# Kernel optimization log

Hardware: AMD Instinct MI355X
Metric: run time of the kernel (lower is better)

The kernel has to match this reference:

```python
import jax, jax.numpy as jnp
import numpy as np

N_HEADS = 16


def setup_inputs() -> dict:
    key = jax.random.key(0)
    k1, k2, k3 = jax.random.split(key, 3)
    d = 1024
    x = jax.random.normal(k1, (8, 1024, d), dtype=jnp.float32)
    w_qkv = jax.random.normal(k2, (d, 3 * d), dtype=jnp.float32) * (1.0 / np.sqrt(d))
    w_out = jax.random.normal(k3, (d, d), dtype=jnp.float32) * (1.0 / np.sqrt(d))
    b_out = jnp.zeros((d,), dtype=jnp.float32)
    return {"x": x, "w_qkv": w_qkv, "w_out": w_out, "b_out": b_out}


def reference(x, w_qkv, w_out, b_out):
    a, b, c = x.shape
    h = N_HEADS
    hd = c // h
    scale = 1.0 / (c ** 0.5)  # note: 1/sqrt(model_dim), not head_dim
    qkv = (x @ w_qkv).reshape(a, b, 3, h, hd)
    q, k, v = jnp.moveaxis(qkv, 2, 0)          # each (a, b, h, hd)
    q = jnp.swapaxes(q, 1, 2)                  # (a, h, b, hd)
    k = jnp.swapaxes(k, 1, 2)
    v = jnp.swapaxes(v, 1, 2)
    scores = jnp.einsum('ahqd,ahkd->ahqk', q, k) * scale  # (a, h, b, b)
    # Faithful to the source: softmax over dim=1 (the HEADS axis)
    attn = jax.nn.softmax(scores, axis=1)
    out = jnp.einsum('ahqk,ahkd->ahqd', attn, v)           # (a, h, b, hd)
    out = jnp.swapaxes(out, 1, 2).reshape(a, b, c)
    return out @ w_out + b_out
```

## Files before the change

kernel.cpp:

```cpp
#include <hip/hip_runtime.h>
#include <hip/hip_bf16.h>

typedef __attribute__((ext_vector_type(8))) short short8;
typedef __attribute__((ext_vector_type(4))) float f32x4;
typedef __attribute__((ext_vector_type(16))) float f32x16;
typedef __attribute__((ext_vector_type(4))) unsigned uint4v;

#define SC_LOG2E 0.04508422f
#define MFMA32(a, b, c) __builtin_amdgcn_mfma_f32_32x32x16_bf16(a, b, c, 0, 0, 0)

__device__ inline short bf16r(float f) {
    union { float f; unsigned u; } v; v.f = f;
    unsigned r = v.u + 0x7FFFu + ((v.u >> 16) & 1u);
    return (short)(r >> 16);
}
__device__ inline float bflo(unsigned u) {
    union { unsigned u; float f; } v; v.u = u << 16; return v.f;
}
__device__ inline float bfhi(unsigned u) {
    union { unsigned u; float f; } v; v.u = u & 0xffff0000u; return v.f;
}
#if __has_builtin(__builtin_amdgcn_exp2f)
__device__ inline float fexp2(float x) { return __builtin_amdgcn_exp2f(x); }
#else
__device__ inline float fexp2(float x) { return __expf(x * 0.6931471806f); }
#endif
__device__ inline unsigned cvt_pk_bf16(float lo, float hi) {
    unsigned r;
    asm("v_cvt_pk_bf16_f32 %0, %1, %2" : "=v"(r) : "v"(lo), "v"(hi));
    return r;
}
__device__ inline void perm32swap(unsigned& a, unsigned& b) {
    asm("v_permlane32_swap_b32 %0, %1" : "+v"(a), "+v"(b));
}

#define GLOAD_LDS16(gp, lp) __builtin_amdgcn_global_load_lds( \
    (const __attribute__((address_space(1))) unsigned int*)(gp), \
    (__attribute__((address_space(3))) unsigned int*)(lp), 16, 0, 0)

__global__ void castk(const float* __restrict__ in, short* __restrict__ out, int n4) {
    int i = blockIdx.x * 256 + threadIdx.x;
    if (i < n4) {
        float4 v = ((const float4*)in)[i];
        short4 o;
        o.x = bf16r(v.x); o.y = bf16r(v.y); o.z = bf16r(v.z); o.w = bf16r(v.w);
        ((short4*)out)[i] = o;
    }
}

__global__ void tcast(const float* __restrict__ src, short* __restrict__ dst, int R, int C,
                      int nscale, float sfac) {
    __shared__ float tile[32][33];
    int bi = blockIdx.x, bj = blockIdx.y;
    int tx = threadIdx.x & 31, ty = threadIdx.x >> 5;
#pragma unroll
    for (int p = 0; p < 4; p++)
        tile[ty + p * 8][tx] = src[(long)(bi * 32 + ty + p * 8) * C + bj * 32 + tx];
    __syncthreads();
#pragma unroll
    for (int p = 0; p < 4; p++) {
        int n = bj * 32 + ty + p * 8;
        float v = tile[tx][ty + p * 8];
        if (n < nscale) v *= sfac;
        dst[(long)n * R + bi * 32 + tx] = bf16r(v);
    }
}

__global__ void vtrans(const short* __restrict__ qkv, short* __restrict__ Vt) {
    __shared__ short tile[32][33];
    int a = blockIdx.z, bi = blockIdx.x, bj = blockIdx.y;
    int tx = threadIdx.x & 31, ty = threadIdx.x >> 5;
#pragma unroll
    for (int p = 0; p < 4; p++) {
        int k = bi * 32 + ty + p * 8;
        int r = bj * 32 + tx;
        tile[ty + p * 8][tx] = qkv[(long)(a * 1024 + k) * 3072 + 2048 + r];
    }
    __syncthreads();
#pragma unroll
    for (int p = 0; p < 4; p++) {
        int r = bj * 32 + ty + p * 8;
        int k = bi * 32 + tx;
        Vt[(long)a * 1048576 + (long)r * 1024 + k] = tile[tx][ty + p * 8];
    }
}

template<int OUT_BF16>
__global__ __launch_bounds__(256, 2)
void gemm_bt(const short* __restrict__ A, const short* __restrict__ Bt,
             void* __restrict__ Cout, const float* __restrict__ bias,
             int M, int N, int K, int nbx, int cpx, int lda) {
    __shared__ short As[2][128 * 32];
    __shared__ short Bs[2][128 * 32];
    const int wg = blockIdx.x;
    const int lg = (wg & 7) * cpx + (wg >> 3);
    const int bx = lg % nbx, by = lg / nbx;
    const int tid = threadIdx.x, w = tid >> 6, lane = tid & 63;
    const int wr = w >> 1, wc = w & 1;
    const int l15 = lane & 15, lhi = lane >> 4;
    const int m0 = by * 128, n0 = bx * 128;
    f32x4 acc[4][4] = {};
    const int NT = K / 32;

    auto stage = [&](int buf, int t) {
        int k0 = t * 32;
#pragma unroll
        for (int j = 0; j < 2; j++) {
            int chunk = w * 128 + j * 64 + lane;
            int row = chunk >> 2, cc = chunk & 3;
            GLOAD_LDS16(A  + (long)(m0 + row) * lda + k0 + cc * 8, &As[buf][chunk * 8]);
            GLOAD_LDS16(Bt + (long)(n0 + row) * K   + k0 + cc * 8, &Bs[buf][chunk * 8]);
        }
    };

    stage(0, 0);
    __syncthreads();
    int buf = 0;
    for (int t = 0; t < NT; t++) {
        if (t + 1 < NT) stage(buf ^ 1, t + 1);
        short8 af[4], bfr[4];
#pragma unroll
        for (int i = 0; i < 4; i++) {
            af[i]  = *(const short8*)(&As[buf][(wr * 64 + i * 16 + l15) * 32 + lhi * 8]);
            bfr[i] = *(const short8*)(&Bs[buf][(wc * 64 + i * 16 + l15) * 32 + lhi * 8]);
        }
#pragma unroll
        for (int i = 0; i < 4; i++)
#pragma unroll
            for (int j = 0; j < 4; j++)
                acc[i][j] = __builtin_amdgcn_mfma_f32_16x16x32_bf16(af[i], bfr[j], acc[i][j], 0, 0, 0);
        __syncthreads();
        buf ^= 1;
    }
#pragma unroll
    for (int i = 0; i < 4; i++)
#pragma unroll
        for (int j = 0; j < 4; j++)
#pragma unroll
            for (int r = 0; r < 4; r++) {
                int row = m0 + wr * 64 + i * 16 + lhi * 4 + r;
                int col = n0 + wc * 64 + j * 16 + l15;
                float v = acc[i][j][r];
                if (OUT_BF16) ((short*)Cout)[(long)row * N + col] = bf16r(v);
                else          ((float*)Cout)[(long)row * N + col] = v + bias[col];
            }
}

__global__ __launch_bounds__(256, 2)
void dsum_kernel(const short* __restrict__ qkv, unsigned* __restrict__ negL) {
    __shared__ short Qs[2][128 * 64];
    __shared__ short Ks[2][128 * 64];
    const int wg = blockIdx.x;
    const int lg = (wg & 7) * 64 + (wg >> 3);
    const int a = lg >> 6, q0 = ((lg >> 3) & 7) * 128, k0 = (lg & 7) * 128;
    const int tid = threadIdx.x, w = tid >> 6, lane = tid & 63;
    const int wr = w >> 1, wc = w & 1;
    const int l31 = lane & 31, hi = lane >> 5;
    const long qb = (long)a * 3145728;
    f32x16 dacc[2][2] = {};

    auto stage = [&](int buf, int hh) {
#pragma unroll
        for (int j = 0; j < 4; j++) {
            int c = j * 256 + tid;
            int row = c >> 3, cc = (c & 7) ^ (row & 7);
            GLOAD_LDS16(qkv + qb + (long)(q0 + row) * 3072 + hh * 64 + cc * 8,        &Qs[buf][c * 8]);
            GLOAD_LDS16(qkv + qb + (long)(k0 + row) * 3072 + 1024 + hh * 64 + cc * 8, &Ks[buf][c * 8]);
        }
    };

    stage(0, 0);
    __syncthreads();
    int buf = 0;
    for (int hh = 0; hh < 16; hh++) {
        if (hh < 15) stage(buf ^ 1, hh + 1);
        short8 ka[2][4], qf[2][4];
#pragma unroll
        for (int i = 0; i < 2; i++)
#pragma unroll
            for (int dc = 0; dc < 4; dc++) {
                int row = wr * 64 + i * 32 + l31;
                int ph = (dc * 2 + hi) ^ (row & 7);
                ka[i][dc] = *(const short8*)(&Ks[buf][row * 64 + ph * 8]);
            }
#pragma unroll
        for (int j = 0; j < 2; j++)
#pragma unroll
            for (int dc = 0; dc < 4; dc++) {
                int row = wc * 64 + j * 32 + l31;
                int ph = (dc * 2 + hi) ^ (row & 7);
                qf[j][dc] = *(const short8*)(&Qs[buf][row * 64 + ph * 8]);
            }
#pragma unroll
        for (int i = 0; i < 2; i++)
#pragma unroll
            for (int j = 0; j < 2; j++) {
                f32x16 s = {};
#pragma unroll
                for (int dc = 0; dc < 4; dc++)
                    s = MFMA32(ka[i][dc], qf[j][dc], s);
#pragma unroll
                for (int r = 0; r < 16; r++)
                    dacc[i][j][r] += fexp2(s[r]);
            }
        __syncthreads();
        buf ^= 1;
    }
#pragma unroll
    for (int i = 0; i < 2; i++)
#pragma unroll
        for (int j = 0; j < 2; j++) {
            int ktg = (k0 >> 5) + wr * 2 + i;
            int qtg = (q0 >> 5) + wc * 2 + j;
            unsigned pwv[8];
#pragma unroll
            for (int u = 0; u < 8; u++)
                pwv[u] = cvt_pk_bf16(-__log2f(dacc[i][j][2 * u]),
                                     -__log2f(dacc[i][j][2 * u + 1]));
            unsigned* dst = negL + (((long)(a * 32 + ktg) * 32 + qtg) << 9) + lane * 8;
            *(uint4v*)dst       = (uint4v){pwv[0], pwv[1], pwv[2], pwv[3]};
            *(uint4v*)(dst + 4) = (uint4v){pwv[4], pwv[5], pwv[6], pwv[7]};
        }
}

__global__ __launch_bounds__(256, 2)
void attn2_kernel(const short* __restrict__ qkv, const short* __restrict__ Vt,
                  const unsigned* __restrict__ negL, short* __restrict__ ctx) {
    __shared__ short lds[3 * 8192];
    const int wg = blockIdx.x;
    const int lg = (wg & 7) * 64 + (wg >> 3);
    const int a = lg >> 6, h = (lg >> 2) & 15, qblk = lg & 3;
    const int tid = threadIdx.x, w = tid >> 6, lane = tid & 63;
    const int l31 = lane & 31, hi = lane >> 5;
    const int qw = qblk * 256 + w * 64;
    const long qb = (long)a * 3145728;

    short8 qfrag[2][4];
#pragma unroll
    for (int qs = 0; qs < 2; qs++)
#pragma unroll
        for (int dc = 0; dc < 4; dc++)
            qfrag[qs][dc] = *(const short8*)(qkv + qb +
                (long)(qw + qs * 32 + l31) * 3072 + h * 64 + dc * 16 + hi * 8);

    const short* kcol  = qkv + qb + 1024 + h * 64;
    const short* vbase = Vt + (long)a * 1048576 + (long)(h * 64) * 1024;
    const unsigned* lbase = negL + (long)a * 524288 + (qw >> 5) * 512 + lane * 8;

    auto stage = [&](int buf, int t) {
        int k0 = t * 64;
#pragma unroll
        for (int j = 0; j < 2; j++) {
            GLOAD_LDS16(kcol + (long)(k0 + j * 32 + l31) * 3072 + w * 16 + hi * 8,
                        &lds[buf * 8192 + (j * 256 + tid) * 8]);
            int fidx = j * 4 + w, n = fidx >> 1, dt = fidx & 1;
            GLOAD_LDS16(vbase + (long)(dt * 32 + l31) * 1024 + k0 + n * 16 + hi * 8,
                        &lds[buf * 8192 + 4096 + (j * 256 + tid) * 8]);
        }
    };

    f32x16 oacc[2][2] = {};
    stage(0, 0);
    stage(1, 1);
    asm volatile("s_waitcnt vmcnt(4)\ns_barrier" ::: "memory");
    __builtin_amdgcn_sched_barrier(0);

    int bR = 0, bW = 2;
    for (int t = 0; t < 16; t++) {
        uint4v dm[2][2][2];
#pragma unroll
        for (int qs = 0; qs < 2; qs++)
#pragma unroll
            for (int kt = 0; kt < 2; kt++) {
                const unsigned* dp = lbase + (long)(t * 2 + kt) * 16384 + qs * 512;
                dm[qs][kt][0] = *(const uint4v*)dp;
                dm[qs][kt][1] = *(const uint4v*)(dp + 4);
            }
        if (t + 2 < 16) stage(bW, t + 2);

        const short* Kb = &lds[bR * 8192];
        const short* Vb = &lds[bR * 8192 + 4096];
#pragma unroll
        for (int kt = 0; kt < 2; kt++) {
            short8 ka[4];
#pragma unroll
            for (int dc = 0; dc < 4; dc++)
                ka[dc] = *(const short8*)(Kb + ((kt * 4 + dc) * 64 + lane) * 8);

            short8 pf[2][2];
#pragma unroll
            for (int qs = 0; qs < 2; qs++) {
                f32x16 s = {};
                __builtin_amdgcn_s_setprio(1);
#pragma unroll
                for (int dc = 0; dc < 4; dc++)
                    s = MFMA32(ka[dc], qfrag[qs][dc], s);
                __builtin_amdgcn_s_setprio(0);
                unsigned pw[8];
#pragma unroll
                for (int u = 0; u < 8; u++) {
                    unsigned d = dm[qs][kt][u >> 2][u & 3];
                    float e0 = fexp2(s[2 * u]     + bflo(d));
                    float e1 = fexp2(s[2 * u + 1] + bfhi(d));
                    pw[u] = cvt_pk_bf16(e0, e1);
                }
                perm32swap(pw[0], pw[2]); perm32swap(pw[1], pw[3]);
                perm32swap(pw[4], pw[6]); perm32swap(pw[5], pw[7]);
                union { uint4v u; short8 s8; } c0, c1;
                c0.u = (uint4v){pw[0], pw[1], pw[2], pw[3]};
                c1.u = (uint4v){pw[4], pw[5], pw[6], pw[7]};
                pf[qs][0] = c0.s8;
                pf[qs][1] = c1.s8;
            }
            __builtin_amdgcn_s_setprio(1);
#pragma unroll
            for (int dt = 0; dt < 2; dt++)
#pragma unroll
                for (int nn = 0; nn < 2; nn++) {
                    short8 vf = *(const short8*)(Vb + (((kt * 2 + nn) * 2 + dt) * 64 + lane) * 8);
#pragma unroll
                    for (int qs = 0; qs < 2; qs++)
                        oacc[qs][dt] = MFMA32(pf[qs][nn], vf, oacc[qs][dt]);
                }
            __builtin_amdgcn_s_setprio(0);
        }
        asm volatile("s_waitcnt vmcnt(4)\ns_barrier" ::: "memory");
        __builtin_amdgcn_sched_barrier(0);
        bR = (bR == 2) ? 0 : bR + 1;
        bW = (bW == 2) ? 0 : bW + 1;
    }
#pragma unroll
    for (int qs = 0; qs < 2; qs++)
#pragma unroll
        for (int dt = 0; dt < 2; dt++)
#pragma unroll
            for (int r = 0; r < 16; r++) {
                int q = qw + qs * 32 + (r & 3) + 8 * (r >> 2) + 4 * hi;
                int col = h * 64 + dt * 32 + l31;
                ctx[((long)a * 1024 + q) * 3072 + col] = bf16r(oacc[qs][dt][r]);
            }
}

extern "C" void kernel_launch(void* const* d_in, const int* in_sizes, int n_in,
                              void* d_out, int out_size, void* d_ws, size_t ws_size,
                              hipStream_t stream) {
    const float* x     = (const float*)d_in[0];
    const float* w_qkv = (const float*)d_in[1];
    const float* w_out = (const float*)d_in[2];
    const float* b_out = (const float*)d_in[3];
    float* out = (float*)d_out;

    char* ws = (char*)d_ws;
    short* wqkvT   = (short*)(ws);
    unsigned* negL = (unsigned*)(ws);
    short* woT   = (short*)(ws + 33554432);
    short* qkv   = (short*)(ws + 35651584);
    short* Vt    = (short*)(ws + 85983232);
    short* xb    = (short*)(ws + 85983232);
    short* ctx   = qkv + 2048;
    if (ws_size < 109051904u) return;

    castk<<<8192, 256, 0, stream>>>(x, xb, 2097152);
    tcast<<<dim3(32, 96), 256, 0, stream>>>(w_qkv, wqkvT, 1024, 3072, 1024, SC_LOG2E);
    tcast<<<dim3(32, 32), 256, 0, stream>>>(w_out, woT, 1024, 1024, 0, 1.0f);
    gemm_bt<1><<<1536, 256, 0, stream>>>(xb, wqkvT, (void*)qkv, nullptr, 8192, 3072, 1024, 24, 192, 1024);
    vtrans<<<dim3(32, 32, 8), 256, 0, stream>>>(qkv, Vt);
    dsum_kernel<<<512, 256, 0, stream>>>(qkv, negL);
    attn2_kernel<<<512, 256, 0, stream>>>(qkv, Vt, negL, ctx);
    gemm_bt<0><<<512, 256, 0, stream>>>(ctx, woT, (void*)out, b_out, 8192, 1024, 1024, 8, 64, 3072);
}
```

Baseline: 196.1 us.

## Triple-buffer GEMM LDS pipeline with fragment-ordered layout and vmcnt waits

The bf16 GEMM moves from double to triple buffering, prefetching two k-tiles ahead, and waits with partial vmcnt counts plus a raw barrier in place of a full __syncthreads. The LDS tile layout becomes fragment-ordered, so each lane's MFMA operand is a contiguous 16-byte read, which should cut bank conflicts. Launch bounds are raised to 3 blocks per CU and s_setprio is placed around the MFMA block. The costs are more LDS per block (48KB), which may limit occupancy, and fragile hand-written waitcnt logic.

```diff
diff --git a/kernel.cpp b/kernel.cpp
--- a/kernel.cpp
+++ b/kernel.cpp
@@ -86,12 +86,11 @@
 }
 
 template<int OUT_BF16>
-__global__ __launch_bounds__(256, 2)
+__global__ __launch_bounds__(256, 3)
 void gemm_bt(const short* __restrict__ A, const short* __restrict__ Bt,
              void* __restrict__ Cout, const float* __restrict__ bias,
              int M, int N, int K, int nbx, int cpx, int lda) {
-    __shared__ short As[2][128 * 32];
-    __shared__ short Bs[2][128 * 32];
+    __shared__ short lds[3 * 8192];
     const int wg = blockIdx.x;
     const int lg = (wg & 7) * cpx + (wg >> 3);
     const int bx = lg % nbx, by = lg / nbx;
@@ -103,34 +102,45 @@
     const int NT = K / 32;
 
     auto stage = [&](int buf, int t) {
-        int k0 = t * 32;
+        int k0 = t * 32 + lhi * 8;
 #pragma unroll
         for (int j = 0; j < 2; j++) {
-            int chunk = w * 128 + j * 64 + lane;
-            int row = chunk >> 2, cc = chunk & 3;
-            GLOAD_LDS16(A  + (long)(m0 + row) * lda + k0 + cc * 8, &As[buf][chunk * 8]);
-            GLOAD_LDS16(Bt + (long)(n0 + row) * K   + k0 + cc * 8, &Bs[buf][chunk * 8]);
+            int g = w * 2 + j;
+            int row = (g >> 2) * 64 + (g & 3) * 16 + l15;
+            GLOAD_LDS16(A  + (long)(m0 + row) * lda + k0, &lds[buf * 8192 + (g * 64 + lane) * 8]);
+            GLOAD_LDS16(Bt + (long)(n0 + row) * K   + k0, &lds[buf * 8192 + 4096 + (g * 64 + lane) * 8]);
         }
     };
 
     stage(0, 0);
-    __syncthreads();
-    int buf = 0;
+    stage(1, 1);
+    asm volatile("s_waitcnt vmcnt(4)\ns_barrier" ::: "memory");
+    __builtin_amdgcn_sched_barrier(0);
+
+    int bR = 0, bW = 2;
     for (int t = 0; t < NT; t++) {
-        if (t + 1 < NT) stage(buf ^ 1, t + 1);
+        bool issued = (t + 2 < NT);
+        if (issued) stage(bW, t + 2);
+        const short* Ab = &lds[bR * 8192];
+        const short* Bb = &lds[bR * 8192 + 4096];
         short8 af[4], bfr[4];
 #pragma unroll
         for (int i = 0; i < 4; i++) {
-            af[i]  = *(const short8*)(&As[buf][(wr * 64 + i * 16 + l15) * 32 + lhi * 8]);
-            bfr[i] = *(const short8*)(&Bs[buf][(wc * 64 + i * 16 + l15) * 32 + lhi * 8]);
-        }
+            af[i]  = *(const short8*)(Ab + ((wr * 4 + i) * 64 + lane) * 8);
+            bfr[i] = *(const short8*)(Bb + ((wc * 4 + i) * 64 + lane) * 8);
+        }
+        __builtin_amdgcn_s_setprio(1);
 #pragma unroll
         for (int i = 0; i < 4; i++)
 #pragma unroll
             for (int j = 0; j < 4; j++)
                 acc[i][j] = __builtin_amdgcn_mfma_f32_16x16x32_bf16(af[i], bfr[j], acc[i][j], 0, 0, 0);
-        __syncthreads();
-        buf ^= 1;
+        __builtin_amdgcn_s_setprio(0);
+        if (issued) asm volatile("s_waitcnt vmcnt(4)\ns_barrier" ::: "memory");
+        else        asm volatile("s_waitcnt vmcnt(0)\ns_barrier" ::: "memory");
+        __builtin_amdgcn_sched_barrier(0);
+        bR = (bR == 2) ? 0 : bR + 1;
+        bW = (bW == 2) ? 0 : bW + 1;
     }
 #pragma unroll
     for (int i = 0; i < 4; i++)
```

After: 230.3 us. 1.17x slower.
